# Kernel optimization log

Measured on AMD Instinct MI355X. Metric: run time of the kernel, lower is better.

Reference implementation:

```python
import jax, jax.numpy as jnp
import numpy as np

D = 1024  # in_features
H = 16    # head_num

def setup_inputs() -> dict:
    key = jax.random.key(0)
    ks = jax.random.split(key, 11)
    S, B = 2048, 2
    scale = 1.0 / np.sqrt(D)
    inp = {
        'q': jax.random.normal(ks[0], (S, B, D), jnp.float32),
        'k': jax.random.normal(ks[1], (S, B, D), jnp.float32),
        'v': jax.random.normal(ks[2], (S, B, D), jnp.float32),
        'Wq': jax.random.normal(ks[3], (D, D), jnp.float32) * scale,
        'Wk': jax.random.normal(ks[4], (D, D), jnp.float32) * scale,
        'Wv': jax.random.normal(ks[5], (D, D), jnp.float32) * scale,
        'Wo': jax.random.normal(ks[6], (D, D), jnp.float32) * scale,
        'bq': jax.random.normal(ks[7], (D,), jnp.float32) * 0.01,
        'bk': jax.random.normal(ks[8], (D,), jnp.float32) * 0.01,
        'bv': jax.random.normal(ks[9], (D,), jnp.float32) * 0.01,
        'bo': jax.random.normal(ks[10], (D,), jnp.float32) * 0.01,
    }
    return inp

def reference(q, k, v, Wq, Wk, Wv, Wo, bq, bk, bv, bo):
    # q,k,v: (S, B, D) -> (B, S, D)
    q = jnp.transpose(q, (1, 0, 2))
    k = jnp.transpose(k, (1, 0, 2))
    v = jnp.transpose(v, (1, 0, 2))
    # linear + ReLU (torch Linear: x @ W.T + b)
    qh = jax.nn.relu(q @ Wq.T + bq)
    kh = jax.nn.relu(k @ Wk.T + bk)
    vh = jax.nn.relu(v @ Wv.T + bv)
    B, S, _ = qh.shape
    hd = D // H
    # (B, S, H, hd) -> (B, H, S, hd)
    qh = qh.reshape(B, S, H, hd).transpose(0, 2, 1, 3)
    kh = kh.reshape(B, S, H, hd).transpose(0, 2, 1, 3)
    vh = vh.reshape(B, S, H, hd).transpose(0, 2, 1, 3)
    scores = jnp.einsum('bhsd,bhtd->bhst', qh, kh) / np.sqrt(hd).astype(np.float32)
    attn = jax.nn.softmax(scores, axis=-1)
    y = jnp.einsum('bhst,bhtd->bhsd', attn, vh)  # (B, H, S, hd)
    y = y.transpose(0, 2, 1, 3).reshape(B, S, D)
    y = jax.nn.relu(y @ Wo.T + bo)
    return jnp.transpose(y, (1, 0, 2))  # (S, B, D)
```

## Files before the change

### kernel.cpp

```cpp
#include <hip/hip_runtime.h>
#include <stdint.h>

typedef __attribute__((ext_vector_type(8))) short bf8v;
typedef __attribute__((ext_vector_type(4))) float f4v;
typedef __attribute__((ext_vector_type(16))) float f16v;
typedef __attribute__((ext_vector_type(4))) unsigned int u4v;

__device__ __forceinline__ unsigned short f2bf(float f) {
  unsigned int u = __float_as_uint(f);
  u += 0x7fffu + ((u >> 16) & 1u);
  return (unsigned short)(u >> 16);
}

__device__ __forceinline__ float bf2f(unsigned short s) {
  return __uint_as_float((unsigned)s << 16);
}

__device__ __forceinline__ void gload16(const void* g, void* l) {
  __builtin_amdgcn_global_load_lds(
      (__attribute__((address_space(1))) void*)reinterpret_cast<uintptr_t>(g),
      (__attribute__((address_space(3))) void*)reinterpret_cast<uintptr_t>(l),
      16, 0, 0);
}

__device__ __forceinline__ unsigned cvtpk(float lo, float hi) {
  unsigned r;
  asm("v_cvt_pk_bf16_f32 %0, %1, %2" : "=v"(r) : "v"(lo), "v"(hi));
  return r;
}

__global__ __launch_bounds__(256) void cvt_all(
    const float* __restrict__ s0, const float* __restrict__ s1,
    const float* __restrict__ s2, const float* __restrict__ s3,
    const float* __restrict__ s4, const float* __restrict__ s5,
    const float* __restrict__ s6, unsigned short* __restrict__ dst) {
  const size_t NA = (size_t)1 << 22, NW = (size_t)1 << 20;
  size_t i = ((size_t)blockIdx.x * 256 + threadIdx.x) * 8;
  const float* src;
  size_t off;
  if (i < 3 * NA) {
    int a = (int)(i >> 22);
    src = (a == 0) ? s0 : (a == 1) ? s1 : s2;
    off = i & (NA - 1);
  } else {
    size_t j = i - 3 * NA;
    int a = (int)(j >> 20);
    src = (a == 0) ? s3 : (a == 1) ? s4 : (a == 2) ? s5 : s6;
    off = j & (NW - 1);
  }
  const f4v* sp = (const f4v*)(src + off);
  f4v x = sp[0], y = sp[1];
  bf8v r;
  r[0] = (short)f2bf(x[0]); r[1] = (short)f2bf(x[1]);
  r[2] = (short)f2bf(x[2]); r[3] = (short)f2bf(x[3]);
  r[4] = (short)f2bf(y[0]); r[5] = (short)f2bf(y[1]);
  r[6] = (short)f2bf(y[2]); r[7] = (short)f2bf(y[3]);
  *(bf8v*)(dst + i) = r;
}

template <int OMODE, int TN>
__device__ __forceinline__ void gemm_body(
    unsigned short* Al, unsigned short* Bl,
    const unsigned short* __restrict__ A, const unsigned short* __restrict__ W,
    const float* __restrict__ bias, void* __restrict__ out) {
  const int tid = threadIdx.x;
  const int w = tid >> 6, l = tid & 63;
  const int lr = l >> 4, lc = l & 15;
  const int m0 = blockIdx.x * 128, n0 = blockIdx.y * TN;
  const int wr = w >> 1, wc = w & 1;
  const int JW = TN / 32;
  const int BCPW = TN / 64;
  const int BBUF = TN * 32;

  f4v acc[4][JW];
#pragma unroll
  for (int i = 0; i < 4; i++)
#pragma unroll
    for (int j = 0; j < JW; j++) acc[i][j] = (f4v)(0.0f);

  const int NK = 32;
#pragma unroll
  for (int i = 0; i < 2; i++) {
    int chunk = w * 2 + i;
    int e = chunk * 512 + l * 8;
    int r = e >> 5, k = e & 31;
    gload16(A + (size_t)(m0 + r) * 1024 + k, Al + chunk * 512);
  }
#pragma unroll
  for (int i = 0; i < BCPW; i++) {
    int chunk = w * BCPW + i;
    int e = chunk * 512 + l * 8;
    int r = e >> 5, k = e & 31;
    gload16(W + (size_t)(n0 + r) * 1024 + k, Bl + chunk * 512);
  }

  for (int kk = 0; kk < NK; kk++) {
    const int cur = kk & 1;
    __syncthreads();
    if (kk + 1 < NK) {
#pragma unroll
      for (int i = 0; i < 2; i++) {
        int chunk = w * 2 + i;
        int e = chunk * 512 + l * 8;
        int r = e >> 5, k = (kk + 1) * 32 + (e & 31);
        gload16(A + (size_t)(m0 + r) * 1024 + k, Al + (cur ^ 1) * 4096 + chunk * 512);
      }
#pragma unroll
      for (int i = 0; i < BCPW; i++) {
        int chunk = w * BCPW + i;
        int e = chunk * 512 + l * 8;
        int r = e >> 5, k = (kk + 1) * 32 + (e & 31);
        gload16(W + (size_t)(n0 + r) * 1024 + k, Bl + (cur ^ 1) * BBUF + chunk * 512);
      }
    }
    bf8v av[4], bv[JW];
#pragma unroll
    for (int i = 0; i < 4; i++) {
      int row = wr * 64 + i * 16 + lc;
      av[i] = *(const bf8v*)(Al + cur * 4096 + row * 32 + lr * 8);
    }
#pragma unroll
    for (int j = 0; j < JW; j++) {
      int row = wc * (TN / 2) + j * 16 + lc;
      bv[j] = *(const bf8v*)(Bl + cur * BBUF + row * 32 + lr * 8);
    }
#pragma unroll
    for (int i = 0; i < 4; i++)
#pragma unroll
      for (int j = 0; j < JW; j++)
        acc[i][j] = __builtin_amdgcn_mfma_f32_16x16x32_bf16(av[i], bv[j], acc[i][j], 0, 0, 0);
  }

#pragma unroll
  for (int j = 0; j < JW; j++) {
    int n = n0 + wc * (TN / 2) + j * 16 + lc;
    float bj = bias[n];
#pragma unroll
    for (int i = 0; i < 4; i++) {
      int mb = m0 + wr * 64 + i * 16 + lr * 4;
#pragma unroll
      for (int q = 0; q < 4; q++) {
        float val = fmaxf(acc[i][j][q] + bj, 0.0f);
        int m = mb + q;
        if (OMODE == 2) {
          int s = m & 2047, b = m >> 11;
          ((float*)out)[(size_t)(s * 2 + b) * 1024 + n] = val;
        } else {
          int s = m >> 1, b = m & 1;
          int h = n >> 6, d = n & 63;
          if (OMODE == 0)
            ((unsigned short*)out)[((size_t)(b * 16 + h) * 2048 + s) * 64 + d] = f2bf(val);
          else
            ((unsigned short*)out)[((size_t)(b * 16 + h) * 64 + d) * 2048 + s] = f2bf(val);
        }
      }
    }
  }
}

__global__ __launch_bounds__(256) void qkv_gemm(
    const unsigned short* __restrict__ qA, const unsigned short* __restrict__ kA,
    const unsigned short* __restrict__ vA,
    const unsigned short* __restrict__ Wq, const unsigned short* __restrict__ Wk,
    const unsigned short* __restrict__ Wv,
    const float* __restrict__ bq, const float* __restrict__ bk,
    const float* __restrict__ bv,
    unsigned short* __restrict__ Qh, unsigned short* __restrict__ Kh,
    unsigned short* __restrict__ Vt) {
  __shared__ __align__(16) unsigned short Al[2 * 4096];
  __shared__ __align__(16) unsigned short Bl[2 * 4096];
  int z = blockIdx.z;
  if (z == 0)      gemm_body<0, 128>(Al, Bl, qA, Wq, bq, Qh);
  else if (z == 1) gemm_body<0, 128>(Al, Bl, kA, Wk, bk, Kh);
  else             gemm_body<1, 128>(Al, Bl, vA, Wv, bv, Vt);
}

__global__ __launch_bounds__(256) void out_gemm(
    const unsigned short* __restrict__ Y, const unsigned short* __restrict__ Wo,
    const float* __restrict__ bo, float* __restrict__ out) {
  __shared__ __align__(16) unsigned short Al[2 * 4096];
  __shared__ __align__(16) unsigned short Bl[2 * 2048];
  gemm_body<2, 64>(Al, Bl, Y, Wo, bo, out);
}

__global__ __launch_bounds__(256, 4) void attn_kernel(
    const unsigned short* __restrict__ Qh, const unsigned short* __restrict__ Kh,
    const unsigned short* __restrict__ Vt,
    unsigned short* __restrict__ PO, float2* __restrict__ ML) {
  __shared__ __align__(16) unsigned short Kl[2][4096];
  __shared__ __align__(16) unsigned short Vl[2][4096];
  const int tid = threadIdx.x, w = tid >> 6, l = tid & 63;
  const int lo = l & 31, hi = l >> 5;
  const int bh = blockIdx.y;
  const int z = blockIdx.z;
  const int tbeg = z << 10, tend = tbeg + 1024;
  const int q0 = blockIdx.x * 128 + w * 32;
  const size_t qkbase = (size_t)bh * 2048 * 64;
  const size_t vtbase = (size_t)bh * 64 * 2048;
  const float cs = 0.125f * 1.44269504088896341f;

  bf8v qf[4];
#pragma unroll
  for (int c = 0; c < 4; c++)
    qf[c] = *(const bf8v*)(Qh + qkbase + (size_t)(q0 + lo) * 64 + c * 16 + hi * 8);

  f16v oacc[2];
  oacc[0] = (f16v)(0.0f);
  oacc[1] = (f16v)(0.0f);
  float mrun = -1e30f, lrun = 0.0f;

  const int swl = (lo & 7) << 4;
  int akb[4], avb[2][2][2];
#pragma unroll
  for (int c = 0; c < 4; c++) akb[c] = lo * 128 + ((c * 32 + hi * 16) ^ swl);
#pragma unroll
  for (int dt = 0; dt < 2; dt++)
#pragma unroll
    for (int kvh = 0; kvh < 2; kvh++)
#pragma unroll
      for (int kc = 0; kc < 2; kc++)
        avb[dt][kvh][kc] = (dt * 32 + lo) * 128 + ((kvh * 64 + kc * 32 + hi * 16) ^ swl);

  int stE[2], stD[2], stKV[2];
#pragma unroll
  for (int i = 0; i < 2; i++) {
    int o = (w * 2 + i) * 1024 + l * 16;
    int row = o >> 7;
    stE[i] = (o ^ ((row & 7) << 4)) >> 1;
    stD[i] = stE[i] >> 6;
    stKV[i] = stE[i] & 63;
  }
  const char* KlB = (const char*)&Kl[0][0];
  const char* VlB = (const char*)&Vl[0][0];

  auto STAGE = [&](int buf, int t0) {
#pragma unroll
    for (int i = 0; i < 2; i++) {
      gload16(Kh + qkbase + (size_t)t0 * 64 + stE[i], (char*)&Kl[buf][0] + (w * 2 + i) * 1024);
      gload16(Vt + vtbase + (size_t)stD[i] * 2048 + t0 + stKV[i], (char*)&Vl[buf][0] + (w * 2 + i) * 1024);
    }
  };

  auto COMPUTE = [&](int bo) {
#pragma unroll
    for (int kvh = 0; kvh < 2; kvh++) {
      bf8v kf[4];
#pragma unroll
      for (int c = 0; c < 4; c++)
        kf[c] = *(const bf8v*)(KlB + bo + kvh * 4096 + akb[c]);
      f16v sc16 = (f16v)(0.0f);
#pragma unroll
      for (int c = 0; c < 4; c++)
        sc16 = __builtin_amdgcn_mfma_f32_32x32x16_bf16(kf[c], qf[c], sc16, 0, 0, 0);
      bf8v vf[2][2];
#pragma unroll
      for (int dt = 0; dt < 2; dt++)
#pragma unroll
        for (int kc = 0; kc < 2; kc++)
          vf[dt][kc] = *(const bf8v*)(VlB + bo + avb[dt][kvh][kc]);

      float m0a = fmaxf(fmaxf(sc16[0], sc16[1]), sc16[2]);
      float m0b = fmaxf(fmaxf(sc16[3], sc16[4]), sc16[5]);
      float m0c = fmaxf(fmaxf(sc16[6], sc16[7]), sc16[8]);
      float m0d = fmaxf(fmaxf(sc16[9], sc16[10]), sc16[11]);
      float m0e = fmaxf(fmaxf(sc16[12], sc16[13]), sc16[14]);
      float m16 = fmaxf(fmaxf(fmaxf(m0a, m0b), fmaxf(m0c, m0d)), fmaxf(m0e, sc16[15]));
      m16 = fmaxf(m16, __shfl_xor(m16, 32));
      float msc = m16 * cs;
      if (!__all(msc <= mrun + 8.0f)) {
        float mnew = fmaxf(mrun, msc);
        float scl = __builtin_amdgcn_exp2f(mrun - mnew);
        lrun *= scl;
#pragma unroll
        for (int dt = 0; dt < 2; dt++)
#pragma unroll
          for (int r = 0; r < 16; r++) oacc[dt][r] *= scl;
        mrun = mnew;
      }
      float p[16];
      float rs = 0.0f;
#pragma unroll
      for (int r = 0; r < 16; r++) {
        p[r] = __builtin_amdgcn_exp2f(sc16[r] * cs - mrun);
        rs += p[r];
      }
      rs += __shfl_xor(rs, 32);
      lrun += rs;
      bf8v pf[2];
#pragma unroll
      for (int kc = 0; kc < 2; kc++) {
        unsigned a0 = cvtpk(p[kc * 8 + 0], p[kc * 8 + 1]);
        unsigned a1 = cvtpk(p[kc * 8 + 2], p[kc * 8 + 3]);
        unsigned b0 = cvtpk(p[kc * 8 + 4], p[kc * 8 + 5]);
        unsigned b1 = cvtpk(p[kc * 8 + 6], p[kc * 8 + 7]);
        asm("v_permlane32_swap_b32 %0, %1" : "+v"(a0), "+v"(b0));
        asm("v_permlane32_swap_b32 %0, %1" : "+v"(a1), "+v"(b1));
        u4v pw;
        pw[0] = a0; pw[1] = a1; pw[2] = b0; pw[3] = b1;
        pf[kc] = __builtin_bit_cast(bf8v, pw);
      }
#pragma unroll
      for (int dt = 0; dt < 2; dt++)
#pragma unroll
        for (int kc = 0; kc < 2; kc++)
          oacc[dt] = __builtin_amdgcn_mfma_f32_32x32x16_bf16(vf[dt][kc], pf[kc], oacc[dt], 0, 0, 0);
    }
  };

  STAGE(0, tbeg);
  __syncthreads();
#pragma unroll 1
  for (int t0 = tbeg; t0 < tend; t0 += 128) {
    STAGE(1, t0 + 64);
    COMPUTE(0);
    __syncthreads();
    if (t0 + 128 < tend) STAGE(0, t0 + 128);
    COMPUTE(8192);
    __syncthreads();
  }

  {
    int q = q0 + lo;
    size_t prow = (size_t)(z * 32 + bh) * 2048 + q;
    if (hi == 0) ML[prow] = float2{mrun, lrun};
    unsigned short* pp = PO + prow * 64;
#pragma unroll
    for (int dt = 0; dt < 2; dt++)
#pragma unroll
      for (int r = 0; r < 16; r++) {
        int d = dt * 32 + (r & 3) + 8 * (r >> 2) + 4 * hi;
        pp[d] = f2bf(oacc[dt][r]);
      }
  }
}

__global__ __launch_bounds__(256) void combine_kernel(
    const unsigned short* __restrict__ PO, const float2* __restrict__ ML,
    unsigned short* __restrict__ Y) {
  int idx = blockIdx.x * 256 + threadIdx.x;
  int row = idx >> 1, hr = idx & 1;
  int bh = row >> 11, q = row & 2047;
  float2 ml0 = ML[row], ml1 = ML[65536 + row];
  float M = fmaxf(ml0.x, ml1.x);
  float a0 = __builtin_amdgcn_exp2f(ml0.x - M);
  float a1 = __builtin_amdgcn_exp2f(ml1.x - M);
  float L = ml0.y * a0 + ml1.y * a1;
  float s0 = a0 / L, s1 = a1 / L;
  const unsigned short* p0 = PO + (size_t)row * 64 + hr * 32;
  const unsigned short* p1 = PO + ((size_t)65536 + row) * 64 + hr * 32;
  int b = bh >> 4, h = bh & 15;
  unsigned short* yp = Y + (((size_t)(b * 2048 + q)) << 10) + h * 64 + hr * 32;
#pragma unroll
  for (int g = 0; g < 4; g++) {
    bf8v v0 = *(const bf8v*)(p0 + g * 8);
    bf8v v1 = *(const bf8v*)(p1 + g * 8);
    bf8v r;
#pragma unroll
    for (int j = 0; j < 8; j++)
      r[j] = (short)f2bf(bf2f((unsigned short)v0[j]) * s0 +
                         bf2f((unsigned short)v1[j]) * s1);
    *(bf8v*)(yp + g * 8) = r;
  }
}

extern "C" void kernel_launch(void* const* d_in, const int* in_sizes, int n_in,
                              void* d_out, int out_size, void* d_ws, size_t ws_size,
                              hipStream_t stream) {
  const float* q  = (const float*)d_in[0];
  const float* k  = (const float*)d_in[1];
  const float* v  = (const float*)d_in[2];
  const float* Wq = (const float*)d_in[3];
  const float* Wk = (const float*)d_in[4];
  const float* Wv = (const float*)d_in[5];
  const float* Wo = (const float*)d_in[6];
  const float* bq = (const float*)d_in[7];
  const float* bk = (const float*)d_in[8];
  const float* bv = (const float*)d_in[9];
  const float* bo = (const float*)d_in[10];

  const size_t NA = (size_t)4096 * 1024;
  const size_t NW = (size_t)1024 * 1024;
  unsigned short* qA  = (unsigned short*)d_ws;
  unsigned short* kA  = qA  + NA;
  unsigned short* vA  = kA  + NA;
  unsigned short* WqB = vA  + NA;
  unsigned short* WkB = WqB + NW;
  unsigned short* WvB = WkB + NW;
  unsigned short* WoB = WvB + NW;
  unsigned short* Qh  = WoB + NW;
  unsigned short* Kh  = Qh  + NA;
  unsigned short* Vt  = Kh  + NA;
  unsigned short* Y   = Vt  + NA;

  unsigned short* PO = qA;
  float2*         ML = (float2*)vA;

  cvt_all<<<dim3(8192), 256, 0, stream>>>(q, k, v, Wq, Wk, Wv, Wo, qA);

  qkv_gemm<<<dim3(32, 8, 3), 256, 0, stream>>>(qA, kA, vA, WqB, WkB, WvB,
                                               bq, bk, bv, Qh, Kh, Vt);
  attn_kernel<<<dim3(16, 32, 2), 256, 0, stream>>>(Qh, Kh, Vt, PO, ML);
  combine_kernel<<<dim3(512), 256, 0, stream>>>(PO, ML, Y);
  out_gemm<<<dim3(32, 16), 256, 0, stream>>>(Y, WoB, bo, (float*)d_out);
}
```

Measured before the change: 132.3 us.

## Process two 32-row query tiles per wave to reuse K/V LDS fragments

Each attention wave now owns 64 query rows as two 32-row sub-tiles. It reuses every K and V fragment loaded from LDS for both sets of score and output MFMAs, and the grid is halved to match. The per-step cross-half row-sum shuffle is replaced by per-lane partial sums that are combined once at the end with v_permlane32_swap. The row max is exchanged with the same swap, and only inside the rescale branch. The cost is twice the accumulator and Q registers, a launch bound lowered to 2 blocks, and fewer blocks in flight, which reduces occupancy and latency hiding.

```diff
diff --git a/kernel.cpp b/kernel.cpp
--- a/kernel.cpp
+++ b/kernel.cpp
@@ -28,6 +28,8 @@
   asm("v_cvt_pk_bf16_f32 %0, %1, %2" : "=v"(r) : "v"(lo), "v"(hi));
   return r;
 }
+
+#define PAIR_SWAP(x, y) asm("v_permlane32_swap_b32 %0, %1" : "+v"(x), "+v"(y))
 
 __global__ __launch_bounds__(256) void cvt_all(
     const float* __restrict__ s0, const float* __restrict__ s1,
@@ -183,7 +185,7 @@
   gemm_body<2, 64>(Al, Bl, Y, Wo, bo, out);
 }
 
-__global__ __launch_bounds__(256, 4) void attn_kernel(
+__global__ __launch_bounds__(256, 2) void attn_kernel(
     const unsigned short* __restrict__ Qh, const unsigned short* __restrict__ Kh,
     const unsigned short* __restrict__ Vt,
     unsigned short* __restrict__ PO, float2* __restrict__ ML) {
@@ -194,20 +196,23 @@
   const int bh = blockIdx.y;
   const int z = blockIdx.z;
   const int tbeg = z << 10, tend = tbeg + 1024;
-  const int q0 = blockIdx.x * 128 + w * 32;
+  const int q0 = blockIdx.x * 256 + w * 64;
   const size_t qkbase = (size_t)bh * 2048 * 64;
   const size_t vtbase = (size_t)bh * 64 * 2048;
   const float cs = 0.125f * 1.44269504088896341f;
 
-  bf8v qf[4];
-#pragma unroll
-  for (int c = 0; c < 4; c++)
-    qf[c] = *(const bf8v*)(Qh + qkbase + (size_t)(q0 + lo) * 64 + c * 16 + hi * 8);
-
-  f16v oacc[2];
-  oacc[0] = (f16v)(0.0f);
-  oacc[1] = (f16v)(0.0f);
-  float mrun = -1e30f, lrun = 0.0f;
+  bf8v qf[2][4];
+#pragma unroll
+  for (int s = 0; s < 2; s++)
+#pragma unroll
+    for (int c = 0; c < 4; c++)
+      qf[s][c] = *(const bf8v*)(Qh + qkbase + (size_t)(q0 + s * 32 + lo) * 64 + c * 16 + hi * 8);
+
+  f16v oacc[2][2];
+  oacc[0][0] = (f16v)(0.0f); oacc[0][1] = (f16v)(0.0f);
+  oacc[1][0] = (f16v)(0.0f); oacc[1][1] = (f16v)(0.0f);
+  float mrun[2] = {-1e30f, -1e30f};
+  float lrun[2] = {0.0f, 0.0f};
 
   const int swl = (lo & 7) << 4;
   int akb[4], avb[2][2][2];
@@ -248,10 +253,12 @@
 #pragma unroll
       for (int c = 0; c < 4; c++)
         kf[c] = *(const bf8v*)(KlB + bo + kvh * 4096 + akb[c]);
-      f16v sc16 = (f16v)(0.0f);
-#pragma unroll
-      for (int c = 0; c < 4; c++)
-        sc16 = __builtin_amdgcn_mfma_f32_32x32x16_bf16(kf[c], qf[c], sc16, 0, 0, 0);
+      f16v sa = (f16v)(0.0f), sb = (f16v)(0.0f);
+#pragma unroll
+      for (int c = 0; c < 4; c++) {
+        sa = __builtin_amdgcn_mfma_f32_32x32x16_bf16(kf[c], qf[0][c], sa, 0, 0, 0);
+        sb = __builtin_amdgcn_mfma_f32_32x32x16_bf16(kf[c], qf[1][c], sb, 0, 0, 0);
+      }
       bf8v vf[2][2];
 #pragma unroll
       for (int dt = 0; dt < 2; dt++)
@@ -259,51 +266,58 @@
         for (int kc = 0; kc < 2; kc++)
           vf[dt][kc] = *(const bf8v*)(VlB + bo + avb[dt][kvh][kc]);
 
-      float m0a = fmaxf(fmaxf(sc16[0], sc16[1]), sc16[2]);
-      float m0b = fmaxf(fmaxf(sc16[3], sc16[4]), sc16[5]);
-      float m0c = fmaxf(fmaxf(sc16[6], sc16[7]), sc16[8]);
-      float m0d = fmaxf(fmaxf(sc16[9], sc16[10]), sc16[11]);
-      float m0e = fmaxf(fmaxf(sc16[12], sc16[13]), sc16[14]);
-      float m16 = fmaxf(fmaxf(fmaxf(m0a, m0b), fmaxf(m0c, m0d)), fmaxf(m0e, sc16[15]));
-      m16 = fmaxf(m16, __shfl_xor(m16, 32));
-      float msc = m16 * cs;
-      if (!__all(msc <= mrun + 8.0f)) {
-        float mnew = fmaxf(mrun, msc);
-        float scl = __builtin_amdgcn_exp2f(mrun - mnew);
-        lrun *= scl;
+#pragma unroll
+      for (int s = 0; s < 2; s++) {
+        const f16v& sc16 = (s == 0) ? sa : sb;
+        float t0 = fmaxf(fmaxf(sc16[0], sc16[1]), sc16[2]);
+        float t1 = fmaxf(fmaxf(sc16[3], sc16[4]), sc16[5]);
+        float t2 = fmaxf(fmaxf(sc16[6], sc16[7]), sc16[8]);
+        float t3 = fmaxf(fmaxf(sc16[9], sc16[10]), sc16[11]);
+        float t4 = fmaxf(fmaxf(sc16[12], sc16[13]), sc16[14]);
+        float lm = fmaxf(fmaxf(fmaxf(t0, t1), fmaxf(t2, t3)), fmaxf(t4, sc16[15]));
+        float msc = lm * cs;
+        if (!__all(msc <= mrun[s] + 8.0f)) {
+          float x = msc, y = msc;
+          PAIR_SWAP(x, y);
+          float pm = fmaxf(x, y);
+          float mnew = fmaxf(mrun[s], pm);
+          float scl = __builtin_amdgcn_exp2f(mrun[s] - mnew);
+          lrun[s] *= scl;
+#pragma unroll
+          for (int dt = 0; dt < 2; dt++)
+#pragma unroll
+            for (int r = 0; r < 16; r++) oacc[s][dt][r] *= scl;
+          mrun[s] = mnew;
+        }
+        float p[16];
+#pragma unroll
+        for (int r = 0; r < 16; r++)
+          p[r] = __builtin_amdgcn_exp2f(sc16[r] * cs - mrun[s]);
+        float s01 = (p[0] + p[1]) + (p[2] + p[3]);
+        float s23 = (p[4] + p[5]) + (p[6] + p[7]);
+        float s45 = (p[8] + p[9]) + (p[10] + p[11]);
+        float s67 = (p[12] + p[13]) + (p[14] + p[15]);
+        lrun[s] += (s01 + s23) + (s45 + s67);
+        bf8v pf[2];
+#pragma unroll
+        for (int kc = 0; kc < 2; kc++) {
+          unsigned a0 = cvtpk(p[kc * 8 + 0], p[kc * 8 + 1]);
+          unsigned a1 = cvtpk(p[kc * 8 + 2], p[kc * 8 + 3]);
+          unsigned b0 = cvtpk(p[kc * 8 + 4], p[kc * 8 + 5]);
+          unsigned b1 = cvtpk(p[kc * 8 + 6], p[kc * 8 + 7]);
+          PAIR_SWAP(a0, b0);
+          PAIR_SWAP(a1, b1);
+          u4v pw;
+          pw[0] = a0; pw[1] = a1; pw[2] = b0; pw[3] = b1;
+          pf[kc] = __builtin_bit_cast(bf8v, pw);
+        }
 #pragma unroll
         for (int dt = 0; dt < 2; dt++)
 #pragma unroll
-          for (int r = 0; r < 16; r++) oacc[dt][r] *= scl;
-        mrun = mnew;
-      }
-      float p[16];
-      float rs = 0.0f;
-#pragma unroll
-      for (int r = 0; r < 16; r++) {
-        p[r] = __builtin_amdgcn_exp2f(sc16[r] * cs - mrun);
-        rs += p[r];
-      }
-      rs += __shfl_xor(rs, 32);
-      lrun += rs;
-      bf8v pf[2];
-#pragma unroll
-      for (int kc = 0; kc < 2; kc++) {
-        unsigned a0 = cvtpk(p[kc * 8 + 0], p[kc * 8 + 1]);
-        unsigned a1 = cvtpk(p[kc * 8 + 2], p[kc * 8 + 3]);
-        unsigned b0 = cvtpk(p[kc * 8 + 4], p[kc * 8 + 5]);
-        unsigned b1 = cvtpk(p[kc * 8 + 6], p[kc * 8 + 7]);
-        asm("v_permlane32_swap_b32 %0, %1" : "+v"(a0), "+v"(b0));
-        asm("v_permlane32_swap_b32 %0, %1" : "+v"(a1), "+v"(b1));
-        u4v pw;
-        pw[0] = a0; pw[1] = a1; pw[2] = b0; pw[3] = b1;
-        pf[kc] = __builtin_bit_cast(bf8v, pw);
-      }
-#pragma unroll
-      for (int dt = 0; dt < 2; dt++)
-#pragma unroll
-        for (int kc = 0; kc < 2; kc++)
-          oacc[dt] = __builtin_amdgcn_mfma_f32_32x32x16_bf16(vf[dt][kc], pf[kc], oacc[dt], 0, 0, 0);
+          for (int kc = 0; kc < 2; kc++)
+            oacc[s][dt] = __builtin_amdgcn_mfma_f32_32x32x16_bf16(vf[dt][kc], pf[kc],
+                                                                 oacc[s][dt], 0, 0, 0);
+      }
     }
   };
 
@@ -319,17 +333,21 @@
     __syncthreads();
   }
 
-  {
-    int q = q0 + lo;
+#pragma unroll
+  for (int s = 0; s < 2; s++) {
+    float x = lrun[s], y = lrun[s];
+    PAIR_SWAP(x, y);
+    float lt = x + y;
+    int q = q0 + s * 32 + lo;
     size_t prow = (size_t)(z * 32 + bh) * 2048 + q;
-    if (hi == 0) ML[prow] = float2{mrun, lrun};
+    if (hi == 0) ML[prow] = float2{mrun[s], lt};
     unsigned short* pp = PO + prow * 64;
 #pragma unroll
     for (int dt = 0; dt < 2; dt++)
 #pragma unroll
       for (int r = 0; r < 16; r++) {
         int d = dt * 32 + (r & 3) + 8 * (r >> 2) + 4 * hi;
-        pp[d] = f2bf(oacc[dt][r]);
+        pp[d] = f2bf(oacc[s][dt][r]);
       }
   }
 }
@@ -399,7 +417,7 @@
 
   qkv_gemm<<<dim3(32, 8, 3), 256, 0, stream>>>(qA, kA, vA, WqB, WkB, WvB,
                                                bq, bk, bv, Qh, Kh, Vt);
-  attn_kernel<<<dim3(16, 32, 2), 256, 0, stream>>>(Qh, Kh, Vt, PO, ML);
+  attn_kernel<<<dim3(8, 32, 2), 256, 0, stream>>>(Qh, Kh, Vt, PO, ML);
   combine_kernel<<<dim3(512), 256, 0, stream>>>(PO, ML, Y);
   out_gemm<<<dim3(32, 16), 256, 0, stream>>>(Y, WoB, bo, (float*)d_out);
 }
```

Result: faster. 127.7 us (-3.5%).
